# Kernel tuning notes

Hardware: AMD Instinct MI355X
Metric: run time of the kernel (lower is better)

The kernel has to match this reference:

```python
import jax, jax.numpy as jnp
import numpy as np

N_NODES = 100000
N_EDGES = 3200000
EMB = 64
K = 2
NUM_GRAPHS = 512


def setup_inputs() -> dict:
    key = jax.random.key(0)
    ks = jax.random.split(key, 12)
    x = jax.random.normal(ks[0], (N_NODES, EMB), dtype=jnp.float32)
    edge_index = jax.random.randint(ks[1], (2, N_EDGES), 0, N_NODES, dtype=jnp.int64)
    edge_attr = jax.random.normal(ks[2], (N_EDGES, 1), dtype=jnp.float32)
    batch = jnp.sort(jax.random.randint(ks[3], (N_NODES,), 0, NUM_GRAPHS, dtype=jnp.int64))
    s = 1.0 / np.sqrt(EMB)
    wn1 = jax.random.normal(ks[4], (EMB, EMB), dtype=jnp.float32) * s
    bn1 = jnp.zeros((EMB,), jnp.float32)
    wn2 = jax.random.normal(ks[5], (EMB, 1), dtype=jnp.float32) * s
    bn2 = jnp.zeros((1,), jnp.float32)
    wc1 = jax.random.normal(ks[6], (EMB, EMB), dtype=jnp.float32) * s
    bc1 = jnp.zeros((EMB,), jnp.float32)
    wc2 = jax.random.normal(ks[7], (EMB, 2 * K * EMB), dtype=jnp.float32) * s
    bc2 = jnp.zeros((2 * K * EMB,), jnp.float32)
    return dict(x=x, edge_index=edge_index, edge_attr=edge_attr, batch=batch,
                wn1=wn1, bn1=bn1, wn2=wn2, bn2=bn2,
                wc1=wc1, bc1=bc1, wc2=wc2, bc2=bc2)


def reference(x, edge_index, edge_attr, batch, wn1, bn1, wn2, bn2, wc1, bc1, wc2, bc2):
    N, C = x.shape
    alpha = 0.1  # APPNP teleport prob
    # --- APPNP(K=1): gcn_norm with self-loops, one propagation step ---
    loops = jnp.arange(N, dtype=edge_index.dtype)
    src = jnp.concatenate([edge_index[0], loops])
    dst = jnp.concatenate([edge_index[1], loops])
    ones = jnp.ones(src.shape[0], dtype=x.dtype)
    deg = jax.ops.segment_sum(ones, dst, num_segments=N)
    dinv = jnp.where(deg > 0, jax.lax.rsqrt(deg), 0.0)
    norm = dinv[src] * dinv[dst]  # [E+N]
    agg = jax.ops.segment_sum(x[src] * norm[:, None], dst, num_segments=N)
    diffuse_x = (1.0 - alpha) * agg + alpha * x  # [N, C]
    # --- node-wise gate: MLP -> global softmax over all nodes ---
    h = jax.nn.relu(diffuse_x @ wn1 + bn1)
    gamma = h @ wn2 + bn2  # [N, 1]
    gamma = jax.nn.softmax(gamma, axis=0)
    # --- per-graph mean pool + channel-wise MLP ---
    sums = jax.ops.segment_sum(diffuse_x, batch, num_segments=NUM_GRAPHS)
    cnt = jax.ops.segment_sum(jnp.ones((N,), x.dtype), batch, num_segments=NUM_GRAPHS)
    pooled = jnp.where(cnt[:, None] > 0, sums / jnp.maximum(cnt, 1.0)[:, None], 0.0)
    pc = jnp.tanh(jax.nn.relu(pooled @ wc1 + bc1) @ wc2 + bc2)  # [B, 2*K*C]
    alpha_kc = pc[:, : K * C].reshape(NUM_GRAPHS, K, C)
    beta_kc = alpha_kc  # faithful to original bug: beta_kc = alpha_kc.reshape(...)
    # --- per-node affine via kron(alpha_kc, gamma_dense) gathered back to nodes ---
    # alpha_batch[b, n, k, c] = alpha_kc[b, k, c] * gamma_dense[b, n]; mask-gather == index by batch
    g = gamma[:, :, None]  # [N, 1, 1]
    a_node = alpha_kc[batch] * g  # [N, K, C]
    b_node = beta_kc[batch] * g  # [N, K, C]
    out = jnp.max(a_node * x[:, None, :] + b_node, axis=1)  # [N, C]
    return out
```

## Files before the change

### kernel.cpp

```cpp
#include <hip/hip_runtime.h>
#include <cstdint>

#define N_NODES   100000
#define N_EDGES   3200000
#define EMB       64
#define NUM_GRAPHS 512
#define NB        391
#define CAP       9216
#define PCHUNK    8192
#define PBLOCKS   391

__global__ void partition_kernel(const int* __restrict__ ei, int* __restrict__ bcnt,
                                 unsigned* __restrict__ gpairs) {
    __shared__ unsigned sp[PCHUNK];
    __shared__ int scnt[512];
    __shared__ int soff[512];
    __shared__ int scur[512];
    __shared__ int gbase[512];
    __shared__ int s[256];
    int t = threadIdx.x;
    for (int i = t; i < 512; i += 256) scnt[i] = 0;
    __syncthreads();
    int base = blockIdx.x * PCHUNK;
    int lim  = min(N_EDGES - base, PCHUNK);
    for (int k = t; k < lim; k += 256) {
        int d = ei[N_EDGES + base + k];
        atomicAdd(&scnt[d >> 8], 1);
    }
    __syncthreads();
    int a0 = scnt[2 * t], a1 = scnt[2 * t + 1];
    int p = a0 + a1;
    s[t] = p; __syncthreads();
    for (int d = 1; d < 256; d <<= 1) {
        int add = (t >= d) ? s[t - d] : 0;
        __syncthreads();
        s[t] += add;
        __syncthreads();
    }
    int excl = s[t] - p;
    soff[2 * t] = excl;       soff[2 * t + 1] = excl + a0;
    scur[2 * t] = excl;       scur[2 * t + 1] = excl + a0;
    __syncthreads();
    for (int i = t; i < NB; i += 256) gbase[i] = i * CAP + atomicAdd(&bcnt[i], scnt[i]);
    __syncthreads();
    for (int k = t; k < lim; k += 256) {
        int sId = ei[base + k];
        int d   = ei[N_EDGES + base + k];
        int pos = atomicAdd(&scur[d >> 8], 1);
        sp[pos] = (unsigned)sId | ((unsigned)(d & 255) << 17);
    }
    __syncthreads();
    for (int i = t; i < lim; i += 256) {
        unsigned pk = sp[i];
        int lo = 0, hi = NB - 1;
        while (lo < hi) { int mid = (lo + hi + 1) >> 1; if (soff[mid] <= i) lo = mid; else hi = mid - 1; }
        gpairs[gbase[lo] + (i - soff[lo])] = pk;
    }
}

__global__ void bucket_scan_kernel(const int* __restrict__ bcnt, int* __restrict__ bbase) {
    __shared__ int s[512];
    int t = threadIdx.x;
    int v = (t < NB) ? bcnt[t] : 0;
    s[t] = v; __syncthreads();
    for (int d = 1; d < 512; d <<= 1) {
        int add = (t >= d) ? s[t - d] : 0;
        __syncthreads();
        s[t] += add;
        __syncthreads();
    }
    if (t < NB) bbase[t] = s[t] - v;
}

__global__ void bscatter2_kernel(const unsigned* __restrict__ gpairs, const int* __restrict__ bcnt,
                                 const int* __restrict__ bbase, int* __restrict__ ebuf,
                                 int* __restrict__ indeg, int* __restrict__ rowstart,
                                 float* __restrict__ dinv) {
    int b = blockIdx.x, t = threadIdx.x, nlo = b << 8;
    __shared__ int lcnt[256];
    __shared__ int lcur[256];
    __shared__ int s[256];
    lcnt[t] = 0; __syncthreads();
    int cnt = bcnt[b];
    const unsigned* gp = gpairs + (size_t)b * CAP;
    for (int i = t; i < cnt; i += 256) atomicAdd(&lcnt[(gp[i] >> 17) & 255], 1);
    __syncthreads();
    int v = lcnt[t];
    s[t] = v; __syncthreads();
    for (int d = 1; d < 256; d <<= 1) {
        int add = (t >= d) ? s[t - d] : 0;
        __syncthreads();
        s[t] += add;
        __syncthreads();
    }
    int excl = s[t] - v;
    int base = bbase[b];
    int n = nlo + t;
    if (n < N_NODES) {
        indeg[n] = v;
        rowstart[n] = base + excl;
        dinv[n] = rsqrtf((float)(v + 1));
    }
    lcur[t] = base + excl;
    __syncthreads();
    for (int i = t; i < cnt; i += 256) {
        unsigned pk = gp[i];
        int pos = atomicAdd(&lcur[(pk >> 17) & 255], 1);
        ebuf[pos] = (int)(pk & 0x1FFFFu);
    }
}

__global__ void gather_mlp_kernel(const int* __restrict__ ebuf, const int* __restrict__ rowstart,
                                  const int* __restrict__ indeg, const float* __restrict__ dinv,
                                  const float* __restrict__ x, float* __restrict__ dx,
                                  const float* __restrict__ wn1, const float* __restrict__ bn1,
                                  const float* __restrict__ wn2, const float* __restrict__ bn2,
                                  float* __restrict__ gl) {
    __shared__ float wn1s[EMB * EMB];
    __shared__ float bn1s[EMB];
    __shared__ float wn2s[EMB];
    for (int i = threadIdx.x; i < EMB * EMB; i += blockDim.x) wn1s[i] = wn1[i];
    if (threadIdx.x < EMB) { bn1s[threadIdx.x] = bn1[threadIdx.x]; wn2s[threadIdx.x] = wn2[threadIdx.x]; }
    __syncthreads();

    int wid = (blockIdx.x * blockDim.x + threadIdx.x) >> 6;
    if (wid >= N_NODES) return;
    int n = __builtin_amdgcn_readfirstlane(wid);
    int l = threadIdx.x & 63;
    int g = l >> 4;
    int q = l & 15;
    int start = rowstart[n];
    int cnt   = indeg[n];
    float dn  = dinv[n];
    const float4* __restrict__ x4 = (const float4*)x;

    float ax = 0.f, ay = 0.f, az = 0.f, aw = 0.f;
    int j = 0;
    for (; j + 8 <= cnt; j += 8) {
        int sA = ebuf[start + j + g];
        int sB = ebuf[start + j + 4 + g];
        float wA = dinv[sA] * dn;
        float wB = dinv[sB] * dn;
        float4 vA = x4[sA * 16 + q];
        float4 vB = x4[sB * 16 + q];
        ax += vA.x * wA + vB.x * wB;
        ay += vA.y * wA + vB.y * wB;
        az += vA.z * wA + vB.z * wB;
        aw += vA.w * wA + vB.w * wB;
    }
    if (j + 4 <= cnt) {
        int sA = ebuf[start + j + g];
        float wA = dinv[sA] * dn;
        float4 vA = x4[sA * 16 + q];
        ax += vA.x * wA; ay += vA.y * wA; az += vA.z * wA; aw += vA.w * wA;
        j += 4;
    }
    int rem = cnt - j;
    if (g < rem) {
        int sA = ebuf[start + j + g];
        float wA = dinv[sA] * dn;
        float4 vA = x4[sA * 16 + q];
        ax += vA.x * wA; ay += vA.y * wA; az += vA.z * wA; aw += vA.w * wA;
    }
    ax += __shfl_xor(ax, 16); ax += __shfl_xor(ax, 32);
    ay += __shfl_xor(ay, 16); ay += __shfl_xor(ay, 32);
    az += __shfl_xor(az, 16); az += __shfl_xor(az, 32);
    aw += __shfl_xor(aw, 16); aw += __shfl_xor(aw, 32);

    float4 xv = x4[n * 16 + q];
    float s2 = dn * dn;
    float r0 = 0.9f * (ax + xv.x * s2) + 0.1f * xv.x;
    float r1 = 0.9f * (ay + xv.y * s2) + 0.1f * xv.y;
    float r2 = 0.9f * (az + xv.z * s2) + 0.1f * xv.z;
    float r3 = 0.9f * (aw + xv.w * s2) + 0.1f * xv.w;
    if (l < 16) {
        float4 rv; rv.x = r0; rv.y = r1; rv.z = r2; rv.w = r3;
        ((float4*)dx)[n * 16 + q] = rv;
    }

    float rr[4] = {r0, r1, r2, r3};
    float am = bn1s[l];
#pragma unroll
    for (int c = 0; c < EMB; ++c) {
        float b = __shfl(rr[c & 3], c >> 2);
        am += b * wn1s[c * EMB + l];
    }
    float h = fmaxf(am, 0.0f);
    float t = h * wn2s[l];
#pragma unroll
    for (int off = 32; off; off >>= 1) t += __shfl_xor(t, off);
    if (l == 0) gl[n] = t + bn2[0];
}

__global__ void expsum_kernel(const float* __restrict__ gl, float* __restrict__ gsum) {
    __shared__ float red[256];
    float s = 0.0f;
    for (int i = blockIdx.x * blockDim.x + threadIdx.x; i < N_NODES; i += gridDim.x * blockDim.x)
        s += expf(gl[i]);
    red[threadIdx.x] = s; __syncthreads();
    for (int t = 128; t; t >>= 1) {
        if ((int)threadIdx.x < t) red[threadIdx.x] += red[threadIdx.x + t];
        __syncthreads();
    }
    if (threadIdx.x == 0) atomicAdd(gsum, red[0]);
}

__device__ inline int lower_bound_i(const int* a, int n, int key) {
    int lo = 0, hi = n;
    while (lo < hi) {
        int mid = (lo + hi) >> 1;
        if (a[mid] < key) lo = mid + 1; else hi = mid;
    }
    return lo;
}
__global__ void pool_kernel(const float* __restrict__ dx, const int* __restrict__ batch,
                            float* __restrict__ pooled) {
    int g = blockIdx.x;
    int lo = lower_bound_i(batch, N_NODES, g);
    int hi = lower_bound_i(batch, N_NODES, g + 1);
    int lane = threadIdx.x & 63;
    int w = threadIdx.x >> 6;
    float acc = 0.0f;
    for (int n = lo + w; n < hi; n += 4) acc += dx[n * EMB + lane];
    __shared__ float red[4][EMB];
    red[w][lane] = acc; __syncthreads();
    if (threadIdx.x < EMB) {
        float s = red[0][threadIdx.x] + red[1][threadIdx.x] + red[2][threadIdx.x] + red[3][threadIdx.x];
        int cnt = hi - lo;
        pooled[g * EMB + threadIdx.x] = cnt > 0 ? s / (float)cnt : 0.0f;
    }
}

__global__ void graph_mlp_kernel(const float* __restrict__ pooled,
                                 const float* __restrict__ wc1, const float* __restrict__ bc1,
                                 const float* __restrict__ wc2, const float* __restrict__ bc2,
                                 float* __restrict__ alphag) {
    int g = blockIdx.x;
    __shared__ float p[EMB];
    __shared__ float h[EMB];
    if (threadIdx.x < EMB) p[threadIdx.x] = pooled[g * EMB + threadIdx.x];
    __syncthreads();
    if (threadIdx.x < EMB) {
        int j = threadIdx.x;
        float a = bc1[j];
        for (int c = 0; c < EMB; ++c) a += p[c] * wc1[c * EMB + j];
        h[j] = fmaxf(a, 0.0f);
    }
    __syncthreads();
    int o = threadIdx.x;
    float a = bc2[o];
    for (int j = 0; j < EMB; ++j) a += h[j] * wc2[j * 256 + o];
    alphag[g * 128 + o] = tanhf(a);
}

__global__ void final_kernel(const float* __restrict__ x, const int* __restrict__ batch,
                             const float* __restrict__ gl, const float* __restrict__ gsum,
                             const float* __restrict__ alphag, float* __restrict__ out) {
    int n = (blockIdx.x * blockDim.x + threadIdx.x) >> 6;
    if (n >= N_NODES) return;
    int lane = threadIdx.x & 63;
    int g = batch[n];
    float gamma = expf(gl[n]) / gsum[0];
    float a0 = alphag[g * 128 + lane];
    float a1 = alphag[g * 128 + 64 + lane];
    float t = gamma * (x[n * EMB + lane] + 1.0f);
    out[n * EMB + lane] = fmaxf(a0 * t, a1 * t);
}

extern "C" void kernel_launch(void* const* d_in, const int* in_sizes, int n_in,
                              void* d_out, int out_size, void* d_ws, size_t ws_size,
                              hipStream_t stream) {
    const float* x     = (const float*)d_in[0];
    const int*   ei    = (const int*)d_in[1];
    const int*   batch = (const int*)d_in[3];
    const float* wn1 = (const float*)d_in[4];
    const float* bn1 = (const float*)d_in[5];
    const float* wn2 = (const float*)d_in[6];
    const float* bn2 = (const float*)d_in[7];
    const float* wc1 = (const float*)d_in[8];
    const float* bc1 = (const float*)d_in[9];
    const float* wc2 = (const float*)d_in[10];
    const float* bc2 = (const float*)d_in[11];
    float* out = (float*)d_out;

    char* wsb = (char*)d_ws;
    float* dx     = (float*)wsb;
    float* gl     = dx + (size_t)N_NODES * EMB;
    float* dinv   = gl + N_NODES;
    float* pooled = dinv + N_NODES;
    float* alphag = pooled + NUM_GRAPHS * EMB;
    int*   bcnt   = (int*)(alphag + NUM_GRAPHS * 128);
    float* gsum   = (float*)(bcnt + 512);
    int*   bbase  = (int*)(gsum + 1);
    int*   indeg  = bbase + 512;
    int*   rowstart = indeg + N_NODES;
    int*   ebuf   = rowstart + N_NODES;
    unsigned* gpairs = (unsigned*)dx;

    hipMemsetAsync(bcnt, 0, 513 * sizeof(int), stream);
    partition_kernel<<<PBLOCKS, 256, 0, stream>>>(ei, bcnt, gpairs);
    bucket_scan_kernel<<<1, 512, 0, stream>>>(bcnt, bbase);
    bscatter2_kernel<<<NB, 256, 0, stream>>>(gpairs, bcnt, bbase, ebuf, indeg, rowstart, dinv);
    gather_mlp_kernel<<<(N_NODES * 64) / 256, 256, 0, stream>>>(ebuf, rowstart, indeg, dinv, x, dx,
                                                                wn1, bn1, wn2, bn2, gl);
    expsum_kernel<<<256, 256, 0, stream>>>(gl, gsum);
    pool_kernel<<<NUM_GRAPHS, 256, 0, stream>>>(dx, batch, pooled);
    graph_mlp_kernel<<<NUM_GRAPHS, 128, 0, stream>>>(pooled, wc1, bc1, wc2, bc2, alphag);
    final_kernel<<<N_NODES / 4, 256, 0, stream>>>(x, batch, gl, gsum, alphag, out);
}
```

Before: 324.0 us.

## Gather neighbor features from bf16 channel-sliced copy and split node MLP

```diff
diff --git a/kernel.cpp b/kernel.cpp
--- a/kernel.cpp
+++ b/kernel.cpp
@@ -9,6 +9,22 @@
 #define CAP       9216
 #define PCHUNK    8192
 #define PBLOCKS   391
+
+__device__ __forceinline__ float bflo(unsigned u) { return __uint_as_float(u << 16); }
+__device__ __forceinline__ float bfhi(unsigned u) { return __uint_as_float(u & 0xFFFF0000u); }
+__device__ __forceinline__ unsigned rne_bf16(float f) {
+    unsigned b = __float_as_uint(f);
+    return (b + 0x7FFFu + ((b >> 16) & 1u)) >> 16;
+}
+
+__global__ void cvt_slice_kernel(const float* __restrict__ x, unsigned* __restrict__ xs) {
+    int i = blockIdx.x * 256 + threadIdx.x;
+    if (i >= N_NODES * 32) return;
+    int n = i >> 5, k = i & 31;
+    float2 f = ((const float2*)x)[i];
+    unsigned u = rne_bf16(f.x) | (rne_bf16(f.y) << 16);
+    xs[(size_t)(k >> 2) * N_NODES * 4 + n * 4 + (k & 3)] = u;
+}
 
 __global__ void partition_kernel(const int* __restrict__ ei, int* __restrict__ bcnt,
                                  unsigned* __restrict__ gpairs) {
@@ -110,6 +126,61 @@
     }
 }
 
+__global__ void slice_gather(const int* __restrict__ ebuf, const int* __restrict__ rowstart,
+                             const int* __restrict__ indeg, const float* __restrict__ dinv,
+                             const unsigned* __restrict__ xs, const float* __restrict__ x,
+                             float* __restrict__ dx) {
+    int slice = blockIdx.x & 7;
+    int node  = ((blockIdx.x >> 3) << 2) + (threadIdx.x >> 6);
+    if (node >= N_NODES) return;
+    int l = threadIdx.x & 63;
+    int q = l & 3, e = l >> 2;
+    int start = rowstart[node];
+    int cnt   = indeg[node];
+    float dn  = dinv[node];
+    const unsigned* __restrict__ xsl = xs + (size_t)slice * N_NODES * 4;
+
+    float a0 = 0.f, a1 = 0.f, b0 = 0.f, b1 = 0.f;
+    int j = 0;
+    for (; j + 32 <= cnt; j += 32) {
+        int sA = ebuf[start + j + e];
+        int sB = ebuf[start + j + 16 + e];
+        float wA = dinv[sA] * dn;
+        float wB = dinv[sB] * dn;
+        unsigned uA = xsl[sA * 4 + q];
+        unsigned uB = xsl[sB * 4 + q];
+        a0 += bflo(uA) * wA; a1 += bfhi(uA) * wA;
+        b0 += bflo(uB) * wB; b1 += bfhi(uB) * wB;
+    }
+    if (j + 16 <= cnt) {
+        int sA = ebuf[start + j + e];
+        float wA = dinv[sA] * dn;
+        unsigned uA = xsl[sA * 4 + q];
+        a0 += bflo(uA) * wA; a1 += bfhi(uA) * wA;
+        j += 16;
+    }
+    if (e < cnt - j) {
+        int sA = ebuf[start + j + e];
+        float wA = dinv[sA] * dn;
+        unsigned uA = xsl[sA * 4 + q];
+        b0 += bflo(uA) * wA; b1 += bfhi(uA) * wA;
+    }
+    a0 += b0; a1 += b1;
+    a0 += __shfl_xor(a0, 4);  a1 += __shfl_xor(a1, 4);
+    a0 += __shfl_xor(a0, 8);  a1 += __shfl_xor(a1, 8);
+    a0 += __shfl_xor(a0, 16); a1 += __shfl_xor(a1, 16);
+    a0 += __shfl_xor(a0, 32); a1 += __shfl_xor(a1, 32);
+
+    if (l < 4) {
+        float2 xv = *(const float2*)&x[(size_t)node * EMB + slice * 8 + 2 * l];
+        float s2 = dn * dn;
+        float2 r;
+        r.x = 0.9f * (a0 + xv.x * s2) + 0.1f * xv.x;
+        r.y = 0.9f * (a1 + xv.y * s2) + 0.1f * xv.y;
+        *(float2*)&dx[(size_t)node * EMB + slice * 8 + 2 * l] = r;
+    }
+}
+
 __global__ void gather_mlp_kernel(const int* __restrict__ ebuf, const int* __restrict__ rowstart,
                                   const int* __restrict__ indeg, const float* __restrict__ dinv,
                                   const float* __restrict__ x, float* __restrict__ dx,
@@ -177,7 +248,6 @@
         float4 rv; rv.x = r0; rv.y = r1; rv.z = r2; rv.w = r3;
         ((float4*)dx)[n * 16 + q] = rv;
     }
-
     float rr[4] = {r0, r1, r2, r3};
     float am = bn1s[l];
 #pragma unroll
@@ -190,6 +260,33 @@
 #pragma unroll
     for (int off = 32; off; off >>= 1) t += __shfl_xor(t, off);
     if (l == 0) gl[n] = t + bn2[0];
+}
+
+__global__ void node_mlp_kernel(const float* __restrict__ dx,
+                                const float* __restrict__ wn1, const float* __restrict__ bn1,
+                                const float* __restrict__ wn2, const float* __restrict__ bn2,
+                                float* __restrict__ gl) {
+    __shared__ float wn1s[EMB * EMB];
+    __shared__ float bn1s[EMB];
+    __shared__ float wn2s[EMB];
+    for (int i = threadIdx.x; i < EMB * EMB; i += blockDim.x) wn1s[i] = wn1[i];
+    if (threadIdx.x < EMB) { bn1s[threadIdx.x] = bn1[threadIdx.x]; wn2s[threadIdx.x] = wn2[threadIdx.x]; }
+    __syncthreads();
+    int n = (blockIdx.x * blockDim.x + threadIdx.x) >> 6;
+    if (n >= N_NODES) return;
+    int j = threadIdx.x & 63;
+    float rowv = dx[n * EMB + j];
+    float acc = bn1s[j];
+#pragma unroll
+    for (int c = 0; c < EMB; ++c) {
+        float b = __shfl(rowv, c);
+        acc += b * wn1s[c * EMB + j];
+    }
+    float h = fmaxf(acc, 0.0f);
+    float t = h * wn2s[j];
+#pragma unroll
+    for (int off = 32; off; off >>= 1) t += __shfl_xor(t, off);
+    if (j == 0) gl[n] = t + bn2[0];
 }
 
 __global__ void expsum_kernel(const float* __restrict__ gl, float* __restrict__ gsum) {
@@ -295,14 +392,25 @@
     int*   indeg  = bbase + 512;
     int*   rowstart = indeg + N_NODES;
     int*   ebuf   = rowstart + N_NODES;
+    unsigned* xs  = (unsigned*)(ebuf + N_EDGES);
     unsigned* gpairs = (unsigned*)dx;
 
+    size_t need_sliced = (size_t)((char*)(xs + (size_t)N_NODES * EMB / 2) - wsb);
+    int use_sliced = (ws_size >= need_sliced);
+
     hipMemsetAsync(bcnt, 0, 513 * sizeof(int), stream);
+    if (use_sliced)
+        cvt_slice_kernel<<<(N_NODES * 32 + 255) / 256, 256, 0, stream>>>(x, xs);
     partition_kernel<<<PBLOCKS, 256, 0, stream>>>(ei, bcnt, gpairs);
     bucket_scan_kernel<<<1, 512, 0, stream>>>(bcnt, bbase);
     bscatter2_kernel<<<NB, 256, 0, stream>>>(gpairs, bcnt, bbase, ebuf, indeg, rowstart, dinv);
-    gather_mlp_kernel<<<(N_NODES * 64) / 256, 256, 0, stream>>>(ebuf, rowstart, indeg, dinv, x, dx,
-                                                                wn1, bn1, wn2, bn2, gl);
+    if (use_sliced) {
+        slice_gather<<<(N_NODES / 4) * 8, 256, 0, stream>>>(ebuf, rowstart, indeg, dinv, xs, x, dx);
+        node_mlp_kernel<<<(N_NODES * 64) / 256, 256, 0, stream>>>(dx, wn1, bn1, wn2, bn2, gl);
+    } else {
+        gather_mlp_kernel<<<(N_NODES * 64) / 256, 256, 0, stream>>>(ebuf, rowstart, indeg, dinv, x, dx,
+                                                                    wn1, bn1, wn2, bn2, gl);
+    }
     expsum_kernel<<<256, 256, 0, stream>>>(gl, gsum);
     pool_kernel<<<NUM_GRAPHS, 256, 0, stream>>>(dx, batch, pooled);
     graph_mlp_kernel<<<NUM_GRAPHS, 128, 0, stream>>>(pooled, wc1, bc1, wc2, bc2, alphag);
```

After: 530.3 us. 1.64x slower.
